# Performance work log

Hardware: AMD Instinct MI355X
Metric: run time of the kernel (lower is better)

The kernel has to match this reference:

```python
import jax, jax.numpy as jnp
import numpy as np

B, N, DIN, DOUT, H = 4, 2048, 512, 512, 8
HD = DOUT // H


def setup_inputs() -> dict:
    key = jax.random.key(0)
    ks = jax.random.split(key, 8)
    x = jax.random.normal(ks[0], (B, N, DIN), dtype=jnp.float32)
    mask = jax.random.randint(ks[1], (B, 1, N, N), 0, 2, dtype=jnp.int32)
    s = 1.0 / np.sqrt(DIN)
    Wq = jax.random.uniform(ks[2], (DOUT, DIN), jnp.float32, -s, s)
    Wk = jax.random.uniform(ks[3], (DOUT, DIN), jnp.float32, -s, s)
    Wv = jax.random.uniform(ks[4], (DOUT, DIN), jnp.float32, -s, s)
    bq = jax.random.uniform(ks[5], (DOUT,), jnp.float32, -s, s)
    bk = jax.random.uniform(ks[6], (DOUT,), jnp.float32, -s, s)
    bv = jax.random.uniform(ks[7], (DOUT,), jnp.float32, -s, s)
    return {"x": x, "Wq": Wq, "bq": bq, "Wk": Wk, "bk": bk, "Wv": Wv, "bv": bv, "mask": mask}


def reference(x, Wq, bq, Wk, bk, Wv, bv, mask):
    b, n, _ = x.shape
    # torch Linear: y = x @ W.T + b ; split heads -> [b, h, n, hd]
    def proj(W, bias):
        y = jnp.einsum('bnd,od->bno', x, W) + bias
        return y.reshape(b, n, H, HD).transpose(0, 2, 1, 3)
    Q, K, V = proj(Wq, bq), proj(Wk, bk), proj(Wv, bv)
    scores = jnp.einsum('bhnd,bhmd->bhnm', Q, K) / np.sqrt(HD).astype(np.float32)
    scores = jnp.where(mask == 0, jnp.float32(-1e9), scores)
    attn = jax.nn.softmax(scores, axis=-1)
    ctx = jnp.einsum('bhnm,bhmd->bhnd', attn, V)
    ctx = ctx.transpose(0, 2, 1, 3).reshape(b, n, DOUT)
    return jax.nn.elu(ctx)
```

## Files before the change

### kernel.cpp

```cpp
#include <hip/hip_runtime.h>
#include <math.h>
#include <stdint.h>

#define CB 4
#define CN 2048
#define CDIN 512
#define CDOUT 512
#define CH 8
#define CHD 64
#define CM (CB * CN)
#define CBH (CB * CH)
#define NKT (CN / 64)

typedef _Float16 f16x8 __attribute__((ext_vector_type(8)));
typedef _Float16 f16x4 __attribute__((ext_vector_type(4)));
typedef float    f32x4 __attribute__((ext_vector_type(4)));

#define QSCALE 0.1803368801111204f

__global__ __launch_bounds__(256) void cvt_kernel(
    const float* __restrict__ s0, _Float16* __restrict__ d0, int n0,
    const float* __restrict__ s1, _Float16* __restrict__ d1, int n1,
    const float* __restrict__ s2, _Float16* __restrict__ d2, int n2,
    const float* __restrict__ s3, _Float16* __restrict__ d3, int n3)
{
    const float* s; _Float16* d; int n;
    if (blockIdx.y == 0)      { s = s0; d = d0; n = n0; }
    else if (blockIdx.y == 1) { s = s1; d = d1; n = n1; }
    else if (blockIdx.y == 2) { s = s2; d = d2; n = n2; }
    else                      { s = s3; d = d3; n = n3; }
    int i = (blockIdx.x * 256 + threadIdx.x) * 8;
    const int stride = gridDim.x * 256 * 8;
    for (; i < n; i += stride) {
        float4 a = *(const float4*)&s[i];
        float4 b = *(const float4*)&s[i + 4];
        f16x8 h = {(_Float16)a.x, (_Float16)a.y, (_Float16)a.z, (_Float16)a.w,
                   (_Float16)b.x, (_Float16)b.y, (_Float16)b.z, (_Float16)b.w};
        *(f16x8*)&d[i] = h;
    }
}

__global__ __launch_bounds__(256) void maskbits_kernel(
    const int* __restrict__ mask, unsigned long long* __restrict__ mbits)
{
    const int idx = blockIdx.x * 256 + threadIdx.x;
    const int* src = mask + (size_t)idx * 64;
    unsigned long long m = 0;
    #pragma unroll
    for (int c = 0; c < 16; ++c) {
        int4 v = *(const int4*)&src[c * 4];
        unsigned long long bits = (v.x ? 1ull : 0ull) | (v.y ? 2ull : 0ull) |
                                  (v.z ? 4ull : 0ull) | (v.w ? 8ull : 0ull);
        m |= bits << (c * 4);
    }
    mbits[idx] = m;
}

__global__ __launch_bounds__(256) void proj_kernel(
    const _Float16* __restrict__ xh,
    const _Float16* __restrict__ Wqh, const float* __restrict__ bq,
    const _Float16* __restrict__ Wkh, const float* __restrict__ bk,
    const _Float16* __restrict__ Wvh, const float* __restrict__ bv,
    _Float16* __restrict__ Qf, _Float16* __restrict__ Kf, _Float16* __restrict__ Vt)
{
    const int z = blockIdx.z;
    const _Float16* W; const float* bias;
    if (z == 0)      { W = Wqh; bias = bq; }
    else if (z == 1) { W = Wkh; bias = bk; }
    else             { W = Wvh; bias = bv; }

    __shared__ _Float16 Xs[128][72];
    __shared__ _Float16 Ws[128][72];

    const int tid  = threadIdx.x;
    const int m0   = blockIdx.x * 128;
    const int o0   = blockIdx.y * 128;
    const int lane = tid & 63, w = tid >> 6;
    const int il   = lane & 15, quad = lane >> 4;
    const int srow = tid >> 3, kc = (tid & 7) * 8;

    f32x4 acc[2][8] = {};
    f16x8 xr[4], wr[4];

    #pragma unroll
    for (int i = 0; i < 4; ++i) {
        xr[i] = *(const f16x8*)&xh[(size_t)(m0 + srow + i * 32) * CDIN + kc];
        wr[i] = *(const f16x8*)&W[(size_t)(o0 + srow + i * 32) * CDIN + kc];
    }

    for (int k0 = 0; k0 < CDIN; k0 += 64) {
        #pragma unroll
        for (int i = 0; i < 4; ++i) {
            *(f16x8*)&Xs[srow + i * 32][kc] = xr[i];
            *(f16x8*)&Ws[srow + i * 32][kc] = wr[i];
        }
        __syncthreads();

        if (k0 + 64 < CDIN) {
            #pragma unroll
            for (int i = 0; i < 4; ++i) {
                xr[i] = *(const f16x8*)&xh[(size_t)(m0 + srow + i * 32) * CDIN + k0 + 64 + kc];
                wr[i] = *(const f16x8*)&W[(size_t)(o0 + srow + i * 32) * CDIN + k0 + 64 + kc];
            }
        }

        #pragma unroll
        for (int dh = 0; dh < 2; ++dh) {
            f16x8 A0 = *(const f16x8*)&Xs[w * 32 + il][dh * 32 + quad * 8];
            f16x8 A1 = *(const f16x8*)&Xs[w * 32 + 16 + il][dh * 32 + quad * 8];
            #pragma unroll
            for (int s = 0; s < 8; ++s) {
                f16x8 Bv = *(const f16x8*)&Ws[s * 16 + il][dh * 32 + quad * 8];
                acc[0][s] = __builtin_amdgcn_mfma_f32_16x16x32_f16(A0, Bv, acc[0][s], 0, 0, 0);
                acc[1][s] = __builtin_amdgcn_mfma_f32_16x16x32_f16(A1, Bv, acc[1][s], 0, 0, 0);
            }
        }
        __syncthreads();
    }

    const int b  = m0 / CN;
    const int nb = m0 & (CN - 1);
    #pragma unroll
    for (int s = 0; s < 8; ++s) {
        const int o  = o0 + s * 16 + il;
        const int h  = o >> 6, d = o & 63;
        const int bh = b * CH + h;
        const float bval = bias[o];
        if (z < 2) {
            _Float16* dst = (z == 0) ? Qf : Kf;
            const float sc = (z == 0) ? QSCALE : 1.0f;
            #pragma unroll
            for (int mi = 0; mi < 2; ++mi) {
                #pragma unroll
                for (int r = 0; r < 4; ++r) {
                    int n = nb + w * 32 + mi * 16 + quad * 4 + r;
                    dst[((size_t)bh * CN + n) * CHD + d] =
                        (_Float16)((acc[mi][s][r] + bval) * sc);
                }
            }
        } else {
            #pragma unroll
            for (int mi = 0; mi < 2; ++mi) {
                int n0 = nb + w * 32 + mi * 16 + quad * 4;
                f16x4 pv = {(_Float16)(acc[mi][s][0] + bval),
                            (_Float16)(acc[mi][s][1] + bval),
                            (_Float16)(acc[mi][s][2] + bval),
                            (_Float16)(acc[mi][s][3] + bval)};
                *(f16x4*)&Vt[((size_t)bh * CHD + d) * CN + n0] = pv;
            }
        }
    }
}

__global__ __launch_bounds__(256) void attn_kernel(
    const _Float16* __restrict__ Qf, const _Float16* __restrict__ Kf,
    const _Float16* __restrict__ Vt, const unsigned long long* __restrict__ mbits,
    float* __restrict__ out)
{
    __shared__ _Float16 Ks[2][64][72];
    __shared__ _Float16 Vs[2][64][72];
    __shared__ _Float16 Ps[4][32][72];

    const int tid  = threadIdx.x;
    const int q0   = blockIdx.x * 128;
    const int bh   = blockIdx.y;
    const int b    = bh >> 3, h = bh & 7;
    const int lane = tid & 63, w = tid >> 6;
    const int il   = lane & 15, quad = lane >> 4;
    const int srow = tid >> 2, sc0 = (tid & 3) * 16;

    const _Float16* Qb = Qf + (size_t)bh * CN * CHD;
    const _Float16* Kb = Kf + (size_t)bh * CN * CHD;
    const _Float16* Vb = Vt + (size_t)bh * CHD * CN;

    const int qg0 = q0 + w * 32 + il;
    const int qg1 = qg0 + 16;
    const unsigned long long* mrow0 = mbits + ((size_t)b * CN + qg0) * NKT;
    const unsigned long long* mrow1 = mbits + ((size_t)b * CN + qg1) * NKT;

    f16x8 Qa0 = *(const f16x8*)&Qb[(size_t)qg0 * CHD + quad * 8];
    f16x8 Qa1 = *(const f16x8*)&Qb[(size_t)qg0 * CHD + 32 + quad * 8];
    f16x8 Qa2 = *(const f16x8*)&Qb[(size_t)qg1 * CHD + quad * 8];
    f16x8 Qa3 = *(const f16x8*)&Qb[(size_t)qg1 * CHD + 32 + quad * 8];

    const f16x8 ones = {1.f16, 1.f16, 1.f16, 1.f16, 1.f16, 1.f16, 1.f16, 1.f16};

    f32x4 oacc0[4] = {}, oacc1[4] = {};
    f32x4 lacc0 = {}, lacc1 = {};

    uint4 kA, kB, vA, vB; unsigned long long mn0, mn1;
    {
        const _Float16* kp = &Kb[(size_t)srow * CHD + sc0];
        const _Float16* vp = &Vb[(size_t)srow * CN + sc0];
        kA = *(const uint4*)kp; kB = *(const uint4*)(kp + 8);
        vA = *(const uint4*)vp; vB = *(const uint4*)(vp + 8);
        mn0 = mrow0[0]; mn1 = mrow1[0];
    }
    *(uint4*)&Ks[0][srow][sc0] = kA; *(uint4*)&Ks[0][srow][sc0 + 8] = kB;
    *(uint4*)&Vs[0][srow][sc0] = vA; *(uint4*)&Vs[0][srow][sc0 + 8] = vB;
    __syncthreads();

    for (int kt = 0; kt < NKT; ++kt) {
        const int cur = kt & 1;
        const unsigned long long mc0 = mn0, mc1 = mn1;

        if (kt < NKT - 1) {
            const _Float16* kp = &Kb[(size_t)((kt + 1) * 64 + srow) * CHD + sc0];
            const _Float16* vp = &Vb[(size_t)srow * CN + (kt + 1) * 64 + sc0];
            kA = *(const uint4*)kp; kB = *(const uint4*)(kp + 8);
            vA = *(const uint4*)vp; vB = *(const uint4*)(vp + 8);
            mn0 = mrow0[kt + 1]; mn1 = mrow1[kt + 1];
        }

        f32x4 st0[4] = {}, st1[4] = {};
        #pragma unroll
        for (int s = 0; s < 4; ++s) {
            f16x8 A0 = *(const f16x8*)&Ks[cur][s * 16 + il][quad * 8];
            f16x8 A1 = *(const f16x8*)&Ks[cur][s * 16 + il][32 + quad * 8];
            st0[s] = __builtin_amdgcn_mfma_f32_16x16x32_f16(A0, Qa0, st0[s], 0, 0, 0);
            st0[s] = __builtin_amdgcn_mfma_f32_16x16x32_f16(A1, Qa1, st0[s], 0, 0, 0);
            st1[s] = __builtin_amdgcn_mfma_f32_16x16x32_f16(A0, Qa2, st1[s], 0, 0, 0);
            st1[s] = __builtin_amdgcn_mfma_f32_16x16x32_f16(A1, Qa3, st1[s], 0, 0, 0);
        }

        const uint32_t m0lo = (uint32_t)mc0, m0hi = (uint32_t)(mc0 >> 32);
        const uint32_t m1lo = (uint32_t)mc1, m1hi = (uint32_t)(mc1 >> 32);
        #pragma unroll
        for (int s = 0; s < 4; ++s) {
            const uint32_t mm0 = (s < 2) ? m0lo : m0hi;
            const uint32_t mm1 = (s < 2) ? m1lo : m1hi;
            const int base = (s & 1) * 16 + quad * 4;
            f16x4 p0, p1;
            #pragma unroll
            for (int r = 0; r < 4; ++r) {
                float s0v = ((mm0 >> (base + r)) & 1u) ? st0[s][r] : -1e9f;
                float s1v = ((mm1 >> (base + r)) & 1u) ? st1[s][r] : -1e9f;
                p0[r] = (_Float16)__builtin_amdgcn_exp2f(s0v);
                p1[r] = (_Float16)__builtin_amdgcn_exp2f(s1v);
            }
            *(f16x4*)&Ps[w][il][s * 16 + quad * 4]      = p0;
            *(f16x4*)&Ps[w][16 + il][s * 16 + quad * 4] = p1;
        }

        f16x8 Pa00 = *(const f16x8*)&Ps[w][il][quad * 8];
        f16x8 Pa01 = *(const f16x8*)&Ps[w][il][32 + quad * 8];
        f16x8 Pa10 = *(const f16x8*)&Ps[w][16 + il][quad * 8];
        f16x8 Pa11 = *(const f16x8*)&Ps[w][16 + il][32 + quad * 8];
        #pragma unroll
        for (int s = 0; s < 4; ++s) {
            f16x8 B0 = *(const f16x8*)&Vs[cur][s * 16 + il][quad * 8];
            f16x8 B1 = *(const f16x8*)&Vs[cur][s * 16 + il][32 + quad * 8];
            oacc0[s] = __builtin_amdgcn_mfma_f32_16x16x32_f16(Pa00, B0, oacc0[s], 0, 0, 0);
            oacc0[s] = __builtin_amdgcn_mfma_f32_16x16x32_f16(Pa01, B1, oacc0[s], 0, 0, 0);
            oacc1[s] = __builtin_amdgcn_mfma_f32_16x16x32_f16(Pa10, B0, oacc1[s], 0, 0, 0);
            oacc1[s] = __builtin_amdgcn_mfma_f32_16x16x32_f16(Pa11, B1, oacc1[s], 0, 0, 0);
        }
        lacc0 = __builtin_amdgcn_mfma_f32_16x16x32_f16(Pa00, ones, lacc0, 0, 0, 0);
        lacc0 = __builtin_amdgcn_mfma_f32_16x16x32_f16(Pa01, ones, lacc0, 0, 0, 0);
        lacc1 = __builtin_amdgcn_mfma_f32_16x16x32_f16(Pa10, ones, lacc1, 0, 0, 0);
        lacc1 = __builtin_amdgcn_mfma_f32_16x16x32_f16(Pa11, ones, lacc1, 0, 0, 0);

        if (kt < NKT - 1) {
            *(uint4*)&Ks[cur ^ 1][srow][sc0] = kA;
            *(uint4*)&Ks[cur ^ 1][srow][sc0 + 8] = kB;
            *(uint4*)&Vs[cur ^ 1][srow][sc0] = vA;
            *(uint4*)&Vs[cur ^ 1][srow][sc0 + 8] = vB;
            __syncthreads();
        }
    }

    #pragma unroll
    for (int s = 0; s < 4; ++s) {
        const int d = h * CHD + s * 16 + il;
        #pragma unroll
        for (int r = 0; r < 4; ++r) {
            int n0 = q0 + w * 32 + quad * 4 + r;
            float c0 = oacc0[s][r] / lacc0[r];
            out[((size_t)b * CN + n0) * CDOUT + d] = c0 > 0.f ? c0 : expm1f(c0);
            int n1 = n0 + 16;
            float c1 = oacc1[s][r] / lacc1[r];
            out[((size_t)b * CN + n1) * CDOUT + d] = c1 > 0.f ? c1 : expm1f(c1);
        }
    }
}

extern "C" void kernel_launch(void* const* d_in, const int* in_sizes, int n_in,
                              void* d_out, int out_size, void* d_ws, size_t ws_size,
                              hipStream_t stream) {
    const float* x    = (const float*)d_in[0];
    const float* Wq   = (const float*)d_in[1];
    const float* bq   = (const float*)d_in[2];
    const float* Wk   = (const float*)d_in[3];
    const float* bk   = (const float*)d_in[4];
    const float* Wv   = (const float*)d_in[5];
    const float* bv   = (const float*)d_in[6];
    const int*   mask = (const int*)d_in[7];
    float* out = (float*)d_out;

    const size_t nx = (size_t)CM * CDIN;
    const size_t nw = (size_t)CDOUT * CDIN;
    const size_t nt = (size_t)CBH * CN * CHD;
    _Float16* xh  = (_Float16*)d_ws;
    _Float16* wqh = xh + nx;
    _Float16* wkh = wqh + nw;
    _Float16* wvh = wkh + nw;
    _Float16* Qf  = wvh + nw;
    _Float16* Kf  = Qf + nt;
    _Float16* Vt  = Kf + nt;
    unsigned long long* mbits = (unsigned long long*)(Vt + nt);

    cvt_kernel<<<dim3(2048, 4), 256, 0, stream>>>(
        x, xh, (int)nx, Wq, wqh, (int)nw, Wk, wkh, (int)nw, Wv, wvh, (int)nw);
    maskbits_kernel<<<dim3(CB * CN * NKT / 256), 256, 0, stream>>>(mask, mbits);
    proj_kernel<<<dim3(CM / 128, CDOUT / 128, 3), 256, 0, stream>>>(
        xh, wqh, bq, wkh, bk, wvh, bv, Qf, Kf, Vt);
    attn_kernel<<<dim3(CN / 128, CBH), 256, 0, stream>>>(
        Qf, Kf, Vt, mbits, out);
}
```

Before: 224.7 us.

## Fuse prep kernels and stage projection epilogue through LDS for coalesced stores

```diff
diff --git a/kernel.cpp b/kernel.cpp
--- a/kernel.cpp
+++ b/kernel.cpp
@@ -18,42 +18,44 @@
 
 #define QSCALE 0.1803368801111204f
 
-__global__ __launch_bounds__(256) void cvt_kernel(
-    const float* __restrict__ s0, _Float16* __restrict__ d0, int n0,
-    const float* __restrict__ s1, _Float16* __restrict__ d1, int n1,
-    const float* __restrict__ s2, _Float16* __restrict__ d2, int n2,
-    const float* __restrict__ s3, _Float16* __restrict__ d3, int n3)
-{
-    const float* s; _Float16* d; int n;
-    if (blockIdx.y == 0)      { s = s0; d = d0; n = n0; }
-    else if (blockIdx.y == 1) { s = s1; d = d1; n = n1; }
-    else if (blockIdx.y == 2) { s = s2; d = d2; n = n2; }
-    else                      { s = s3; d = d3; n = n3; }
-    int i = (blockIdx.x * 256 + threadIdx.x) * 8;
-    const int stride = gridDim.x * 256 * 8;
-    for (; i < n; i += stride) {
-        float4 a = *(const float4*)&s[i];
-        float4 b = *(const float4*)&s[i + 4];
-        f16x8 h = {(_Float16)a.x, (_Float16)a.y, (_Float16)a.z, (_Float16)a.w,
-                   (_Float16)b.x, (_Float16)b.y, (_Float16)b.z, (_Float16)b.w};
-        *(f16x8*)&d[i] = h;
-    }
-}
-
-__global__ __launch_bounds__(256) void maskbits_kernel(
+#define PB_X  2048
+#define PB_WQ 2176
+#define PB_WK 2304
+#define PB_WV 2432
+#define PB_MB 3456
+
+__global__ __launch_bounds__(256) void prep_kernel(
+    const float* __restrict__ x,  _Float16* __restrict__ xh,
+    const float* __restrict__ Wq, _Float16* __restrict__ wqh,
+    const float* __restrict__ Wk, _Float16* __restrict__ wkh,
+    const float* __restrict__ Wv, _Float16* __restrict__ wvh,
     const int* __restrict__ mask, unsigned long long* __restrict__ mbits)
 {
-    const int idx = blockIdx.x * 256 + threadIdx.x;
-    const int* src = mask + (size_t)idx * 64;
-    unsigned long long m = 0;
-    #pragma unroll
-    for (int c = 0; c < 16; ++c) {
-        int4 v = *(const int4*)&src[c * 4];
-        unsigned long long bits = (v.x ? 1ull : 0ull) | (v.y ? 2ull : 0ull) |
-                                  (v.z ? 4ull : 0ull) | (v.w ? 8ull : 0ull);
-        m |= bits << (c * 4);
-    }
-    mbits[idx] = m;
+    const int bx = blockIdx.x;
+    if (bx >= PB_WV) {
+        const int idx = (bx - PB_WV) * 256 + threadIdx.x;
+        const int* src = mask + (size_t)idx * 64;
+        unsigned long long m = 0;
+        #pragma unroll
+        for (int c = 0; c < 16; ++c) {
+            int4 v = *(const int4*)&src[c * 4];
+            unsigned long long bits = (v.x ? 1ull : 0ull) | (v.y ? 2ull : 0ull) |
+                                      (v.z ? 4ull : 0ull) | (v.w ? 8ull : 0ull);
+            m |= bits << (c * 4);
+        }
+        mbits[idx] = m;
+        return;
+    }
+    const float* s; _Float16* d; int i;
+    if (bx < PB_X)       { s = x;  d = xh;  i = bx * 2048 + threadIdx.x * 8; }
+    else if (bx < PB_WQ) { s = Wq; d = wqh; i = (bx - PB_X)  * 2048 + threadIdx.x * 8; }
+    else if (bx < PB_WK) { s = Wk; d = wkh; i = (bx - PB_WQ) * 2048 + threadIdx.x * 8; }
+    else                 { s = Wv; d = wvh; i = (bx - PB_WK) * 2048 + threadIdx.x * 8; }
+    float4 a = *(const float4*)&s[i];
+    float4 b = *(const float4*)&s[i + 4];
+    f16x8 h = {(_Float16)a.x, (_Float16)a.y, (_Float16)a.z, (_Float16)a.w,
+               (_Float16)b.x, (_Float16)b.y, (_Float16)b.z, (_Float16)b.w};
+    *(f16x8*)&d[i] = h;
 }
 
 __global__ __launch_bounds__(256) void proj_kernel(
@@ -69,8 +71,7 @@
     else if (z == 1) { W = Wkh; bias = bk; }
     else             { W = Wvh; bias = bv; }
 
-    __shared__ _Float16 Xs[128][72];
-    __shared__ _Float16 Ws[128][72];
+    __shared__ _Float16 SM[2 * 128 * 72];
 
     const int tid  = threadIdx.x;
     const int m0   = blockIdx.x * 128;
@@ -91,8 +92,8 @@
     for (int k0 = 0; k0 < CDIN; k0 += 64) {
         #pragma unroll
         for (int i = 0; i < 4; ++i) {
-            *(f16x8*)&Xs[srow + i * 32][kc] = xr[i];
-            *(f16x8*)&Ws[srow + i * 32][kc] = wr[i];
+            *(f16x8*)&SM[(srow + i * 32) * 72 + kc] = xr[i];
+            *(f16x8*)&SM[9216 + (srow + i * 32) * 72 + kc] = wr[i];
         }
         __syncthreads();
 
@@ -106,13 +107,22 @@
 
         #pragma unroll
         for (int dh = 0; dh < 2; ++dh) {
-            f16x8 A0 = *(const f16x8*)&Xs[w * 32 + il][dh * 32 + quad * 8];
-            f16x8 A1 = *(const f16x8*)&Xs[w * 32 + 16 + il][dh * 32 + quad * 8];
-            #pragma unroll
-            for (int s = 0; s < 8; ++s) {
-                f16x8 Bv = *(const f16x8*)&Ws[s * 16 + il][dh * 32 + quad * 8];
-                acc[0][s] = __builtin_amdgcn_mfma_f32_16x16x32_f16(A0, Bv, acc[0][s], 0, 0, 0);
-                acc[1][s] = __builtin_amdgcn_mfma_f32_16x16x32_f16(A1, Bv, acc[1][s], 0, 0, 0);
+            f16x8 X0 = *(const f16x8*)&SM[(w * 32 + il) * 72 + dh * 32 + quad * 8];
+            f16x8 X1 = *(const f16x8*)&SM[(w * 32 + 16 + il) * 72 + dh * 32 + quad * 8];
+            if (z < 2) {
+                #pragma unroll
+                for (int s = 0; s < 8; ++s) {
+                    f16x8 Wv_ = *(const f16x8*)&SM[9216 + (s * 16 + il) * 72 + dh * 32 + quad * 8];
+                    acc[0][s] = __builtin_amdgcn_mfma_f32_16x16x32_f16(Wv_, X0, acc[0][s], 0, 0, 0);
+                    acc[1][s] = __builtin_amdgcn_mfma_f32_16x16x32_f16(Wv_, X1, acc[1][s], 0, 0, 0);
+                }
+            } else {
+                #pragma unroll
+                for (int s = 0; s < 8; ++s) {
+                    f16x8 Wv_ = *(const f16x8*)&SM[9216 + (s * 16 + il) * 72 + dh * 32 + quad * 8];
+                    acc[0][s] = __builtin_amdgcn_mfma_f32_16x16x32_f16(X0, Wv_, acc[0][s], 0, 0, 0);
+                    acc[1][s] = __builtin_amdgcn_mfma_f32_16x16x32_f16(X1, Wv_, acc[1][s], 0, 0, 0);
+                }
             }
         }
         __syncthreads();
@@ -120,34 +130,55 @@
 
     const int b  = m0 / CN;
     const int nb = m0 & (CN - 1);
-    #pragma unroll
-    for (int s = 0; s < 8; ++s) {
-        const int o  = o0 + s * 16 + il;
-        const int h  = o >> 6, d = o & 63;
-        const int bh = b * CH + h;
-        const float bval = bias[o];
-        if (z < 2) {
-            _Float16* dst = (z == 0) ? Qf : Kf;
-            const float sc = (z == 0) ? QSCALE : 1.0f;
+    if (z < 2) {
+        const float sc = (z == 0) ? QSCALE : 1.0f;
+        #pragma unroll
+        for (int s = 0; s < 8; ++s) {
             #pragma unroll
             for (int mi = 0; mi < 2; ++mi) {
+                f16x4 pv;
                 #pragma unroll
-                for (int r = 0; r < 4; ++r) {
-                    int n = nb + w * 32 + mi * 16 + quad * 4 + r;
-                    dst[((size_t)bh * CN + n) * CHD + d] =
-                        (_Float16)((acc[mi][s][r] + bval) * sc);
-                }
-            }
-        } else {
+                for (int r = 0; r < 4; ++r)
+                    pv[r] = (_Float16)((acc[mi][s][r] + bias[o0 + s * 16 + quad * 4 + r]) * sc);
+                *(f16x4*)&SM[(w * 32 + mi * 16 + il) * 140 + s * 16 + quad * 4] = pv;
+            }
+        }
+    } else {
+        #pragma unroll
+        for (int s = 0; s < 8; ++s) {
+            const float bval = bias[o0 + s * 16 + il];
             #pragma unroll
             for (int mi = 0; mi < 2; ++mi) {
-                int n0 = nb + w * 32 + mi * 16 + quad * 4;
                 f16x4 pv = {(_Float16)(acc[mi][s][0] + bval),
                             (_Float16)(acc[mi][s][1] + bval),
                             (_Float16)(acc[mi][s][2] + bval),
                             (_Float16)(acc[mi][s][3] + bval)};
-                *(f16x4*)&Vt[((size_t)bh * CHD + d) * CN + n0] = pv;
-            }
+                *(f16x4*)&SM[(s * 16 + il) * 140 + w * 32 + mi * 16 + quad * 4] = pv;
+            }
+        }
+    }
+    __syncthreads();
+
+    const int uu   = tid & 127;
+    const int hseg = tid >> 7;
+    const int bh   = b * CH + (o0 >> 6) + hseg;
+    if (z < 2) {
+        _Float16* dst = ((z == 0) ? Qf : Kf) + ((size_t)bh * CN + nb) * CHD;
+        #pragma unroll
+        for (int k = 0; k < 8; ++k) {
+            int n = k * 16 + (uu >> 3);
+            int d = (uu & 7) * 8;
+            *(f16x8*)&dst[(size_t)n * CHD + d] =
+                *(const f16x8*)&SM[n * 140 + hseg * 64 + d];
+        }
+    } else {
+        _Float16* dst = Vt + (size_t)bh * CHD * CN + nb;
+        #pragma unroll
+        for (int k = 0; k < 8; ++k) {
+            int d = k * 8 + (uu >> 4);
+            int n = (uu & 15) * 8;
+            *(f16x8*)&dst[(size_t)d * CN + n] =
+                *(const f16x8*)&SM[(hseg * 64 + d) * 140 + n];
         }
     }
 }
@@ -309,9 +340,8 @@
     _Float16* Vt  = Kf + nt;
     unsigned long long* mbits = (unsigned long long*)(Vt + nt);
 
-    cvt_kernel<<<dim3(2048, 4), 256, 0, stream>>>(
-        x, xh, (int)nx, Wq, wqh, (int)nw, Wk, wkh, (int)nw, Wv, wvh, (int)nw);
-    maskbits_kernel<<<dim3(CB * CN * NKT / 256), 256, 0, stream>>>(mask, mbits);
+    prep_kernel<<<dim3(PB_MB), 256, 0, stream>>>(
+        x, xh, Wq, wqh, Wk, wkh, Wv, wvh, mask, mbits);
     proj_kernel<<<dim3(CM / 128, CDOUT / 128, 3), 256, 0, stream>>>(
         xh, wqh, bq, wkh, bk, wvh, bv, Qf, Kf, Vt);
     attn_kernel<<<dim3(CN / 128, CBH), 256, 0, stream>>>(
```

After: 230.0 us. 1.02x slower.
